# Performance work log

Measured on AMD Instinct MI355X. Metric: run time of the kernel, lower is better.

Reference implementation:

```python
import jax, jax.numpy as jnp
import numpy as np

C = 1.0      # base manifold curvature (Lorentz c)
C_E = 1.0    # expert manifold curvature (all experts init to c=1.0)
K = 1        # n_activated_experts (top-k)
SCALE = 2.0  # LResNet scale for shared-expert combine
EPS = 1e-8


def _lorentz_swiglu(x, W1, W3, W2, c_mid, c_out, prescale):
    """LorentzExpert / LorentzFeedForward: SwiGLU on space coords with Lorentz time lift.
    x: [T, D] (full Lorentz vector). W1,W3: [I-1, D]; W2: [D-1, I]. Returns [T, D]."""
    if prescale:
        x = x * np.float32(np.sqrt(C_E / C))  # x * sqrt(c_expert / c)
    s1 = jax.nn.silu(x @ W1.T)                 # [T, I-1] w1(x, return_space=True)
    s3 = x @ W3.T                              # [T, I-1] w3(x, return_space=True)
    sp = s1 * s3                               # gated space part
    t = jnp.sqrt(jnp.clip((sp * sp).sum(-1, keepdims=True) + c_mid, EPS))
    h = jnp.concatenate([t, sp], axis=-1)      # [T, I] point on expert manifold
    o = h @ W2.T                               # [T, D-1] w2 space output
    ot = jnp.sqrt(jnp.clip((o * o).sum(-1, keepdims=True) + c_out, EPS))
    return jnp.concatenate([ot, o], axis=-1)   # [T, D] on base manifold


def setup_inputs() -> dict:
    key = jax.random.key(0)
    ks = jax.random.split(key, 9)
    T, D, E, I = 2048, 1024, 8, 1024
    x = jax.random.normal(ks[0], (T, D), jnp.float32)
    gate_w = jax.random.normal(ks[1], (E, D - 1), jnp.float32) / np.sqrt(D - 1)
    gate_b = jax.random.normal(ks[2], (E,), jnp.float32) * 0.01
    W1 = jax.random.normal(ks[3], (E, I - 1, D), jnp.float32) / np.sqrt(D)
    W3 = jax.random.normal(ks[4], (E, I - 1, D), jnp.float32) / np.sqrt(D)
    W2 = jax.random.normal(ks[5], (E, D - 1, I), jnp.float32) / np.sqrt(I)
    Ws1 = jax.random.normal(ks[6], (I - 1, D), jnp.float32) / np.sqrt(D)
    Ws3 = jax.random.normal(ks[7], (I - 1, D), jnp.float32) / np.sqrt(D)
    Ws2 = jax.random.normal(ks[8], (D - 1, I), jnp.float32) / np.sqrt(I)
    return {"x": x, "gate_w": gate_w, "gate_b": gate_b, "W1": W1, "W3": W3,
            "W2": W2, "Ws1": Ws1, "Ws3": Ws3, "Ws2": Ws2}


def reference(x, gate_w, gate_b, W1, W3, W2, Ws1, Ws3, Ws2):
    T, D = x.shape
    E = gate_w.shape[0]
    # ---- Gate (softmax scoring, n_groups == 1, route_scale == 1.0) ----
    logits = x[:, 1:] @ gate_w.T                                    # [T, E]
    scores = jax.nn.softmax(logits.astype(jnp.float32), axis=-1)
    biased = scores + gate_b                                        # bias only affects routing
    _, idx = jax.lax.top_k(biased, K)                               # [T, K]
    weights = jnp.take_along_axis(scores, idx, axis=-1).astype(x.dtype)  # [T, K]
    # dense per-token expert gate weights [T, E]
    oh = jax.nn.one_hot(idx, E, dtype=x.dtype)                      # [T, K, E]
    gw = (oh * weights[..., None]).sum(axis=1)                      # [T, E]
    # ---- y init: project(zeros) -> [sqrt(c), 0, ..., 0] ----
    y0 = jnp.concatenate([jnp.full((T, 1), np.sqrt(C), x.dtype),
                          jnp.zeros((T, D - 1), x.dtype)], axis=-1)
    # ---- routed experts (dense reference: every expert on every token, masked combine) ----
    e_out = jax.vmap(lambda w1, w3, w2: _lorentz_swiglu(x, w1, w3, w2, C_E, C, True))(W1, W3, W2)  # [E, T, D]
    y = y0 + jnp.einsum('te,etd->td', gw, e_out)
    # ---- shared expert (LorentzFeedForward, stays on base manifold) ----
    z = _lorentz_swiglu(x, Ws1, Ws3, Ws2, C, C, False)
    # ---- LResNet weighted sum: normalize (z + scale*y) back to manifold ----
    comb = z + SCALE * y
    li = (comb[:, 1:] ** 2).sum(-1, keepdims=True) - comb[:, :1] ** 2  # Lorentz inner <comb,comb>
    out = np.float32(np.sqrt(C)) * comb / jnp.sqrt(jnp.clip(jnp.abs(li), EPS))
    return out
```

## Files before the change

### kernel.cpp

```cpp
#include <hip/hip_runtime.h>

typedef __bf16 bf16;
typedef __attribute__((ext_vector_type(8))) __bf16 bf16x8;
typedef __attribute__((ext_vector_type(4))) float floatx4;

#define TOK 2048
#define DD  1024
#define NE  8
#define S1MAX 48
#define S2MAX 80

#define MFMA16(A,B,C) __builtin_amdgcn_mfma_f32_16x16x32_bf16(A,B,C,0,0,0)

__device__ __forceinline__ void load_lds16(const bf16* g, bf16* l) {
  __builtin_amdgcn_global_load_lds(
      (const __attribute__((address_space(1))) void*)g,
      (__attribute__((address_space(3))) void*)l, 16, 0, 0);
}

#define WBAR(N) asm volatile("s_waitcnt vmcnt(" #N ")\n\ts_barrier" ::: "memory")
#define BARO    asm volatile("s_barrier" ::: "memory")

__device__ __forceinline__ uint4 pack_bf8(float4 a, float4 b) {
  union { bf16 h[8]; uint4 u; } p;
  p.h[0] = (bf16)a.x; p.h[1] = (bf16)a.y; p.h[2] = (bf16)a.z; p.h[3] = (bf16)a.w;
  p.h[4] = (bf16)b.x; p.h[5] = (bf16)b.y; p.h[6] = (bf16)b.z; p.h[7] = (bf16)b.w;
  return p.u;
}

#define NCVT (8*2046 + 2046 + 8*1023 + 1023)
__global__ __launch_bounds__(128) void convert_kernel(
    const float* __restrict__ W1, const float* __restrict__ W3,
    const float* __restrict__ W2, const float* __restrict__ Ws1,
    const float* __restrict__ Ws3, const float* __restrict__ Ws2,
    bf16* __restrict__ w13, bf16* __restrict__ ws13,
    bf16* __restrict__ w2b, bf16* __restrict__ ws2b)
{
  const int r = blockIdx.x, tid = threadIdx.x;
  const float* src; bf16* dst;
  if (r < 8 * 2046) {
    const int e = r / 2046, q = r % 2046;
    src = ((q & 1) ? W3 : W1) + ((size_t)e * 1023 + (q >> 1)) * 1024;
    dst = w13 + (size_t)r * 1024;
// ... 57 lines not shown
    for (int e = 0; e < NE; ++e) lg[e] = red[0][e] + red[1][e] + red[2][e] + red[3][e];
    float m = lg[0];
    for (int e = 1; e < NE; ++e) m = fmaxf(m, lg[e]);
    float ex[NE], s = 0.f;
    for (int e = 0; e < NE; ++e) { ex[e] = expf(lg[e] - m); s += ex[e]; }
    const float inv = 1.f / s;
    int best = 0; float bb = ex[0] * inv + gate_b[0];
    for (int e = 1; e < NE; ++e) {
      const float b = ex[e] * inv + gate_b[e];
      if (b > bb) { bb = b; best = e; }
    }
    eidx[t] = best;
    ewgt[t] = ex[best] * inv;
  }
}

__global__ __launch_bounds__(256) void route_kernel(
    const int* __restrict__ eidx, int* __restrict__ perm,
    int* __restrict__ pos_of, int4* __restrict__ wl1, int* __restrict__ n1,
    int4* __restrict__ wl2, int* __restrict__ n2)
{
  __shared__ int cnt[NE], off[NE], bas[NE + 1];
  const int tid = threadIdx.x;
  if (tid < NE) cnt[tid] = 0;
  __syncthreads();
  for (int t = tid; t < TOK; t += 256) atomicAdd(&cnt[eidx[t]], 1);
  __syncthreads();
  if (tid == 0) {
    int run = 0;
    for (int e = 0; e < NE; ++e) { bas[e] = run; off[e] = run; run += cnt[e]; }
    bas[NE] = run;
    int n = 0;
    for (int e = 0; e < NE; ++e)
      for (int r0 = 0; r0 < cnt[e]; r0 += 128) {
        int rows = cnt[e] - r0; if (rows > 128) rows = 128;
        wl1[n++] = make_int4(bas[e] + r0, rows, e, 0);
      }
    for (int r0 = 0; r0 < TOK; r0 += 128) wl1[n++] = make_int4(r0, 128, NE, 0);
    *n1 = n;
    n = 0;
    for (int e = 0; e < NE; ++e)
      for (int r0 = 0; r0 < cnt[e]; r0 += 64) {
        int rows = cnt[e] - r0; if (rows > 64) rows = 64;
        wl2[n++] = make_int4(bas[e] + r0, rows, e, 0);
      }
    for (int r0 = 0; r0 < TOK; r0 += 64) wl2[n++] = make_int4(r0, 64, NE, 0);
    *n2 = n;
  }
  __syncthreads();
  for (int t = tid; t < TOK; t += 256) {
    const int e = eidx[t];
    const int p = atomicAdd(&off[e], 1);
    perm[p] = t;
    pos_of[t] = p;
  }
}

__global__ __launch_bounds__(256) void mlp1_kernel(
    const bf16* __restrict__ x_bf, const bf16* __restrict__ w13,
    const bf16* __restrict__ ws13,
    const int* __restrict__ perm, const int4* __restrict__ wl,
    const int* __restrict__ wl_n,
    bf16* __restrict__ h_r, bf16* __restrict__ h_s,
    float* __restrict__ ss_r, float* __restrict__ ss_z)
{
  const int bid = blockIdx.x;
  const int slot = bid >> 4, nt = bid & 15;
  if (slot >= *wl_n) return;
  const int4 wle = wl[slot];
  const int mbase = wle.x, rows = wle.y, eid = wle.z;
  const int tid = threadIdx.x;
  const bool routed = (eid < NE);
  const bf16* bmat = routed ? w13 + (size_t)eid * 2046 * 1024 : ws13;
  bf16* hbuf  = routed ? h_r : h_s;
  float* ssbuf = routed ? ss_r : ss_z;

  __shared__ __align__(16) bf16 As[2][128 * 64];
  __shared__ __align__(16) bf16 Bs[2][128 * 64];
  __shared__ int toks[128];
  if (tid < 128) {
    int r = tid < rows ? tid : rows - 1;
    toks[tid] = routed ? perm[mbase + r] : (mbase + r);
  }
  __syncthreads();

  const int wid = tid >> 6, lane = tid & 63;
  const int srow = lane >> 3;
  const int kbg  = (lane & 7) ^ (srow & 7);
  const bf16 *aG0, *aG1, *aG2, *aG3, *bG0, *bG1, *bG2, *bG3;
  int aL0o, aL1o, aL2o, aL3o, bL0o, bL1o, bL2o, bL3o;
  {
    const int r0 = wid * 32;
    aG0 = x_bf + (size_t)toks[r0 +  0 + srow] * 1024 + kbg * 8;
    aG1 = x_bf + (size_t)toks[r0 +  8 + srow] * 1024 + kbg * 8;
    aG2 = x_bf + (size_t)toks[r0 + 16 + srow] * 1024 + kbg * 8;
    aG3 = x_bf + (size_t)toks[r0 + 24 + srow] * 1024 + kbg * 8;
    aL0o = (r0 +  0) * 64; aL1o = (r0 +  8) * 64;
    aL2o = (r0 + 16) * 64; aL3o = (r0 + 24) * 64;
    int b0 = nt * 128 + r0 + 0 + srow;  if (b0 > 2045) b0 = 2045;
    int b1 = nt * 128 + r0 + 8 + srow;  if (b1 > 2045) b1 = 2045;
    int b2 = nt * 128 + r0 + 16 + srow; if (b2 > 2045) b2 = 2045;
    int b3 = nt * 128 + r0 + 24 + srow; if (b3 > 2045) b3 = 2045;
    bG0 = bmat + (size_t)b0 * 1024 + kbg * 8;
    bG1 = bmat + (size_t)b1 * 1024 + kbg * 8;
    bG2 = bmat + (size_t)b2 * 1024 + kbg * 8;
    bG3 = bmat + (size_t)b3 * 1024 + kbg * 8;
    bL0o = (r0 +  0) * 64; bL1o = (r0 +  8) * 64;
    bL2o = (r0 + 16) * 64; bL3o = (r0 + 24) * 64;
  }

  const int lrow = lane & 15, quad = lane >> 4, sw = lane & 7;
  const int wrow = (wid >> 1) * 64, wcol = (wid & 1) * 64;
  int aoff[4], boff[4], koff[2];
#pragma unroll
  for (int mi = 0; mi < 4; ++mi) aoff[mi] = (wrow + mi * 16 + lrow) * 64;
#pragma unroll
  for (int ni = 0; ni < 4; ++ni) boff[ni] = (wcol + ni * 16 + lrow) * 64;
#pragma unroll
  for (int kk = 0; kk < 2; ++kk) koff[kk] = ((kk * 4 + quad) ^ sw) * 8;

  const floatx4 fz = {0.f, 0.f, 0.f, 0.f};
  floatx4 acc[4][4];
#pragma unroll
  for (int mi = 0; mi < 4; ++mi)
#pragma unroll
    for (int ni = 0; ni < 4; ++ni) acc[mi][ni] = fz;

#define STAGE1(KE, BUF) { \
    load_lds16(aG0 + (KE), As[BUF] + aL0o); load_lds16(aG1 + (KE), As[BUF] + aL1o); \
    load_lds16(aG2 + (KE), As[BUF] + aL2o); load_lds16(aG3 + (KE), As[BUF] + aL3o); \
    load_lds16(bG0 + (KE), Bs[BUF] + bL0o); load_lds16(bG1 + (KE), Bs[BUF] + bL1o); \
    load_lds16(bG2 + (KE), Bs[BUF] + bL2o); load_lds16(bG3 + (KE), Bs[BUF] + bL3o); }

#define COMP1(BUF) { \
_Pragma("unroll") \
    for (int kk = 0; kk < 2; ++kk) { \
      bf16x8 av[4], bv[4]; \
_Pragma("unroll") \
      for (int mi = 0; mi < 4; ++mi) av[mi] = *(const bf16x8*)(As[BUF] + aoff[mi] + koff[kk]); \
_Pragma("unroll") \
      for (int ni = 0; ni < 4; ++ni) bv[ni] = *(const bf16x8*)(Bs[BUF] + boff[ni] + koff[kk]); \
_Pragma("unroll") \
      for (int mi = 0; mi < 4; ++mi) \
_Pragma("unroll") \
        for (int ni = 0; ni < 4; ++ni) \
          acc[mi][ni] = MFMA16(av[mi], bv[ni], acc[mi][ni]); \
    } }

  STAGE1(0, 0)
  STAGE1(64, 1)
#pragma unroll 1
  for (int t = 0; t < 7; ++t) {
    const int ke = t * 128;
    WBAR(8); COMP1(0) BARO; STAGE1(ke + 128, 0)
    WBAR(8); COMP1(1) BARO; STAGE1(ke + 192, 1)
  }
  WBAR(8); COMP1(0)
  WBAR(0); COMP1(1)
#undef STAGE1
#undef COMP1

#pragma unroll
  for (int mi = 0; mi < 4; ++mi) {
#pragma unroll
    for (int r = 0; r < 4; ++r) {
      const int row = wrow + mi * 16 + quad * 4 + r;
      const bool rowok = row < rows;
      float ssum = 0.f;
#pragma unroll
      for (int ni = 0; ni < 4; ++ni) {
        const float c = acc[mi][ni][r];
        const float partner = __shfl_xor(c, 1);
        const float s1 = (lane & 1) ? partner : c;
        const float s3 = (lane & 1) ? c : partner;
        const float sp = (s1 / (1.f + __expf(-s1))) * s3;
        const int P = (nt * 128 + wcol + ni * 16 + lrow) >> 1;
        const bool ok = rowok && ((lane & 1) == 0) && (P < 1023);
        if (ok) hbuf[(size_t)(mbase + row) * 1024 + 1 + P] = (bf16)sp;
        ssum += ok ? sp * sp : 0.f;
      }
      ssum += __shfl_xor(ssum, 1);
      ssum += __shfl_xor(ssum, 2);
      ssum += __shfl_xor(ssum, 4);
      ssum += __shfl_xor(ssum, 8);
      if (lrow == 0 && rowok) atomicAdd(ssbuf + mbase + row, ssum);
    }
  }
}

__global__ __launch_bounds__(256) void finalize_t_kernel(
    const float* __restrict__ ss_r, const float* __restrict__ ss_z,
    bf16* __restrict__ h_r, bf16* __restrict__ h_s)
{
  const int i = blockIdx.x * 256 + threadIdx.x;
  if (i < TOK) {
    h_r[(size_t)i * 1024] = (bf16)sqrtf(ss_r[i] + 1.0f);
    h_s[(size_t)i * 1024] = (bf16)sqrtf(ss_z[i] + 1.0f);
  }
}

__global__ __launch_bounds__(256) void mlp2_kernel(
    const bf16* __restrict__ h_r, const bf16* __restrict__ h_s,
    const bf16* __restrict__ w2b, const bf16* __restrict__ ws2b,
    const int4* __restrict__ wl, const int* __restrict__ wl_n,
    float* __restrict__ o_r, float* __restrict__ o_s,
    float* __restrict__ ss_or, float* __restrict__ ss_oz)
{
  const int bid = blockIdx.x;
  const int slot = bid >> 3, nt = bid & 7;
  if (slot >= *wl_n) return;
  const int4 wle = wl[slot];
  const int mbase = wle.x, rows = wle.y, eid = wle.z;
  const int tid = threadIdx.x;
  const bool routed = (eid < NE);
  const bf16* abuf = routed ? h_r : h_s;
  const bf16* bmat = routed ? w2b + (size_t)eid * 1023 * 1024 : ws2b;
  float* obuf  = routed ? o_r : o_s;
  float* ssbuf = routed ? ss_or : ss_oz;
  const int n0 = nt * 128;

  __shared__ __align__(16) bf16 As[2][64 * 64];
  __shared__ __align__(16) bf16 Bs[2][128 * 64];

  const int wid = tid >> 6, lane = tid & 63;
  const int srow = lane >> 3;
  const int kbg  = (lane & 7) ^ (srow & 7);
  const bf16 *aG0, *aG1, *bG0, *bG1, *bG2, *bG3;
  int aL0o, aL1o, bL0o, bL1o, bL2o, bL3o;
  {
    int ra0 = wid * 16 + 0 + srow; if (ra0 >= rows) ra0 = rows - 1;
    int ra1 = wid * 16 + 8 + srow; if (ra1 >= rows) ra1 = rows - 1;
    aG0 = abuf + (size_t)(mbase + ra0) * 1024 + kbg * 8;
    aG1 = abuf + (size_t)(mbase + ra1) * 1024 + kbg * 8;
    aL0o = (wid * 16 + 0) * 64;
    aL1o = (wid * 16 + 8) * 64;
    const int r0 = wid * 32;
    int b0 = n0 + r0 + 0 + srow;  if (b0 > 1022) b0 = 1022;
    int b1 = n0 + r0 + 8 + srow;  if (b1 > 1022) b1 = 1022;
    int b2 = n0 + r0 + 16 + srow; if (b2 > 1022) b2 = 1022;
    int b3 = n0 + r0 + 24 + srow; if (b3 > 1022) b3 = 1022;
    bG0 = bmat + (size_t)b0 * 1024 + kbg * 8;
    bG1 = bmat + (size_t)b1 * 1024 + kbg * 8;
    bG2 = bmat + (size_t)b2 * 1024 + kbg * 8;
    bG3 = bmat + (size_t)b3 * 1024 + kbg * 8;
    bL0o = (r0 +  0) * 64; bL1o = (r0 +  8) * 64;
    bL2o = (r0 + 16) * 64; bL3o = (r0 + 24) * 64;
  }

  const int lrow = lane & 15, quad = lane >> 4, sw = lane & 7;
  const int wrow = (wid >> 1) * 32, wcol = (wid & 1) * 64;
  int aoff[2], boff[4], koff[2];
#pragma unroll
  for (int mi = 0; mi < 2; ++mi) aoff[mi] = (wrow + mi * 16 + lrow) * 64;
#pragma unroll
  for (int ni = 0; ni < 4; ++ni) boff[ni] = (wcol + ni * 16 + lrow) * 64;
#pragma unroll
  for (int kk = 0; kk < 2; ++kk) koff[kk] = ((kk * 4 + quad) ^ sw) * 8;

  const floatx4 fz = {0.f, 0.f, 0.f, 0.f};
  floatx4 acc[2][4];
#pragma unroll
  for (int mi = 0; mi < 2; ++mi)
#pragma unroll
    for (int ni = 0; ni < 4; ++ni) acc[mi][ni] = fz;

#define STAGE2(KE, BUF) { \
    load_lds16(aG0 + (KE), As[BUF] + aL0o); load_lds16(aG1 + (KE), As[BUF] + aL1o); \
    load_lds16(bG0 + (KE), Bs[BUF] + bL0o); load_lds16(bG1 + (KE), Bs[BUF] + bL1o); \
    load_lds16(bG2 + (KE), Bs[BUF] + bL2o); load_lds16(bG3 + (KE), Bs[BUF] + bL3o); }

#define COMP2(BUF) { \
_Pragma("unroll") \
    for (int kk = 0; kk < 2; ++kk) { \
      bf16x8 av[2], bv[4]; \
_Pragma("unroll") \
      for (int mi = 0; mi < 2; ++mi) av[mi] = *(const bf16x8*)(As[BUF] + aoff[mi] + koff[kk]); \
_Pragma("unroll") \
      for (int ni = 0; ni < 4; ++ni) bv[ni] = *(const bf16x8*)(Bs[BUF] + boff[ni] + koff[kk]); \
_Pragma("unroll") \
      for (int mi = 0; mi < 2; ++mi) \
_Pragma("unroll") \
        for (int ni = 0; ni < 4; ++ni) \
          acc[mi][ni] = MFMA16(av[mi], bv[ni], acc[mi][ni]); \
    } }

  STAGE2(0, 0)
  STAGE2(64, 1)
#pragma unroll 1
  for (int t = 0; t < 7; ++t) {
    const int ke = t * 128;
    WBAR(6); COMP2(0) BARO; STAGE2(ke + 128, 0)
    WBAR(6); COMP2(1) BARO; STAGE2(ke + 192, 1)
  }
  WBAR(6); COMP2(0)
  WBAR(0); COMP2(1)
#undef STAGE2
#undef COMP2

#pragma unroll
  for (int mi = 0; mi < 2; ++mi) {
#pragma unroll
    for (int r = 0; r < 4; ++r) {
      const int row = wrow + mi * 16 + quad * 4 + r;
      const bool rowok = row < rows;
      float ssum = 0.f;
#pragma unroll
      for (int ni = 0; ni < 4; ++ni) {
        const float v = acc[mi][ni][r];
        const int n = n0 + wcol + ni * 16 + lrow;
        const bool ok = rowok && (n < 1023);
        if (ok) obuf[(size_t)(mbase + row) * 1024 + n] = v;
        ssum += ok ? v * v : 0.f;
      }
      ssum += __shfl_xor(ssum, 1);
      ssum += __shfl_xor(ssum, 2);
      ssum += __shfl_xor(ssum, 4);
      ssum += __shfl_xor(ssum, 8);
      if (lrow == 0 && rowok) atomicAdd(ssbuf + mbase + row, ssum);
    }
  }
}

__global__ __launch_bounds__(256) void combine_kernel(
    const float* __restrict__ o_r, const float* __restrict__ o_s,
    const float* __restrict__ ss_or, const float* __restrict__ ss_oz,
    const int* __restrict__ pos_of, const float* __restrict__ wgt,
    float* __restrict__ out)
{
  const int t = blockIdx.x, tid = threadIdx.x;
  const int p = pos_of[t];
  const float w = wgt[t];
  const float4 oz = ((const float4*)(o_s + (size_t)t * 1024))[tid];
  const float4 oe = ((const float4*)(o_r + (size_t)p * 1024))[tid];
// ... 35 lines not shown
  const float* Ws2    = (const float*)d_in[8];
  float* out = (float*)d_out;

  char* ws = (char*)d_ws;
  size_t off = 0;
  auto alloc = [&](size_t bytes) {
    void* p = ws + off;
    off += (bytes + 255) & ~(size_t)255;
    return p;
  };
  bf16*  x_bf = (bf16*) alloc((size_t)TOK * 1024 * 2);
  bf16*  h_r  = (bf16*) alloc((size_t)TOK * 1024 * 2);
  bf16*  h_s  = (bf16*) alloc((size_t)TOK * 1024 * 2);
  float* o_r  = (float*)alloc((size_t)TOK * 1024 * 4);
  float* o_s  = (float*)alloc((size_t)TOK * 1024 * 4);
  float* ss   = (float*)alloc((size_t)4 * TOK * 4);
  int*   eidx = (int*)  alloc((size_t)TOK * 4);
  float* ewgt = (float*)alloc((size_t)TOK * 4);
  int*   perm = (int*)  alloc((size_t)TOK * 4);
  int*   posf = (int*)  alloc((size_t)TOK * 4);
  int4*  wl1  = (int4*) alloc((size_t)S1MAX * 16);
  int4*  wl2  = (int4*) alloc((size_t)S2MAX * 16);
  int*   wn   = (int*)  alloc(32);
  bf16*  w13  = (bf16*) alloc((size_t)8 * 2046 * 1024 * 2);
  bf16*  ws13 = (bf16*) alloc((size_t)2046 * 1024 * 2);
  bf16*  w2b  = (bf16*) alloc((size_t)8 * 1023 * 1024 * 2);
  bf16*  ws2b = (bf16*) alloc((size_t)1023 * 1024 * 2);

  float* ss_r  = ss;
  float* ss_z  = ss + TOK;
  float* ss_or = ss + 2 * TOK;
  float* ss_oz = ss + 3 * TOK;

  convert_kernel<<<NCVT, 128, 0, stream>>>(W1, W3, W2, Ws1, Ws3, Ws2,
                                           w13, ws13, w2b, ws2b);
  gate_cvt_kernel<<<TOK, 256, 0, stream>>>(x, gate_w, gate_b, x_bf, eidx, ewgt, ss);
  route_kernel<<<1, 256, 0, stream>>>(eidx, perm, posf, wl1, wn, wl2, wn + 1);
  mlp1_kernel<<<S1MAX * 16, 256, 0, stream>>>(x_bf, w13, ws13, perm, wl1, wn,
                                              h_r, h_s, ss_r, ss_z);
  finalize_t_kernel<<<8, 256, 0, stream>>>(ss_r, ss_z, h_r, h_s);
  mlp2_kernel<<<S2MAX * 8, 256, 0, stream>>>(h_r, h_s, w2b, ws2b, wl2, wn + 1,
                                             o_r, o_s, ss_or, ss_oz);
  combine_kernel<<<TOK, 256, 0, stream>>>(o_r, o_s, ss_or, ss_oz, posf, ewgt, out);
}
```

Measured before the change: 251.5 us.

## Switch GEMM mainloops to BK=32 triple-buffered LDS pipeline without swizzle

Both GEMM kernels now stage K tiles of 32 instead of 64 and rotate through three LDS buffers instead of two, so two loads are in flight while one tile is computed. The XOR swizzle on LDS addressing is removed because each row is now only four 16-byte chunks. Each LDS footprint shrinks, which may allow more blocks per CU, but every K step now has half the MFMA work per barrier, which raises synchronisation overhead. Dropping the swizzle risks LDS bank conflicts.

```diff
diff --git a/kernel.cpp b/kernel.cpp
--- a/kernel.cpp
+++ b/kernel.cpp
@@ -175,8 +175,8 @@
   bf16* hbuf  = routed ? h_r : h_s;
   float* ssbuf = routed ? ss_r : ss_z;
 
-  __shared__ __align__(16) bf16 As[2][128 * 64];
-  __shared__ __align__(16) bf16 Bs[2][128 * 64];
+  __shared__ __align__(16) bf16 As[3][128 * 32];
+  __shared__ __align__(16) bf16 Bs[3][128 * 32];
   __shared__ int toks[128];
   if (tid < 128) {
     int r = tid < rows ? tid : rows - 1;
@@ -185,39 +185,29 @@
   __syncthreads();
 
   const int wid = tid >> 6, lane = tid & 63;
-  const int srow = lane >> 3;
-  const int kbg  = (lane & 7) ^ (srow & 7);
-  const bf16 *aG0, *aG1, *aG2, *aG3, *bG0, *bG1, *bG2, *bG3;
-  int aL0o, aL1o, aL2o, aL3o, bL0o, bL1o, bL2o, bL3o;
+  const int srow  = lane >> 2;
+  const int kslot = lane & 3;
+  const bf16 *aG0, *aG1, *bG0, *bG1;
+  int aL0o, aL1o, bL0o, bL1o;
   {
     const int r0 = wid * 32;
-    aG0 = x_bf + (size_t)toks[r0 +  0 + srow] * 1024 + kbg * 8;
-    aG1 = x_bf + (size_t)toks[r0 +  8 + srow] * 1024 + kbg * 8;
-    aG2 = x_bf + (size_t)toks[r0 + 16 + srow] * 1024 + kbg * 8;
-    aG3 = x_bf + (size_t)toks[r0 + 24 + srow] * 1024 + kbg * 8;
-    aL0o = (r0 +  0) * 64; aL1o = (r0 +  8) * 64;
-    aL2o = (r0 + 16) * 64; aL3o = (r0 + 24) * 64;
-    int b0 = nt * 128 + r0 + 0 + srow;  if (b0 > 2045) b0 = 2045;
-    int b1 = nt * 128 + r0 + 8 + srow;  if (b1 > 2045) b1 = 2045;
-    int b2 = nt * 128 + r0 + 16 + srow; if (b2 > 2045) b2 = 2045;
-    int b3 = nt * 128 + r0 + 24 + srow; if (b3 > 2045) b3 = 2045;
-    bG0 = bmat + (size_t)b0 * 1024 + kbg * 8;
-    bG1 = bmat + (size_t)b1 * 1024 + kbg * 8;
-    bG2 = bmat + (size_t)b2 * 1024 + kbg * 8;
-    bG3 = bmat + (size_t)b3 * 1024 + kbg * 8;
-    bL0o = (r0 +  0) * 64; bL1o = (r0 +  8) * 64;
-    bL2o = (r0 + 16) * 64; bL3o = (r0 + 24) * 64;
-  }
-
-  const int lrow = lane & 15, quad = lane >> 4, sw = lane & 7;
+    aG0 = x_bf + (size_t)toks[r0 +  0 + srow] * 1024 + kslot * 8;
+    aG1 = x_bf + (size_t)toks[r0 + 16 + srow] * 1024 + kslot * 8;
+    aL0o = (r0 +  0) * 32; aL1o = (r0 + 16) * 32;
+    int b0 = nt * 128 + r0 +  0 + srow; if (b0 > 2045) b0 = 2045;
+    int b1 = nt * 128 + r0 + 16 + srow; if (b1 > 2045) b1 = 2045;
+    bG0 = bmat + (size_t)b0 * 1024 + kslot * 8;
+    bG1 = bmat + (size_t)b1 * 1024 + kslot * 8;
+    bL0o = (r0 +  0) * 32; bL1o = (r0 + 16) * 32;
+  }
+
+  const int lrow = lane & 15, quad = lane >> 4;
   const int wrow = (wid >> 1) * 64, wcol = (wid & 1) * 64;
-  int aoff[4], boff[4], koff[2];
-#pragma unroll
-  for (int mi = 0; mi < 4; ++mi) aoff[mi] = (wrow + mi * 16 + lrow) * 64;
-#pragma unroll
-  for (int ni = 0; ni < 4; ++ni) boff[ni] = (wcol + ni * 16 + lrow) * 64;
-#pragma unroll
-  for (int kk = 0; kk < 2; ++kk) koff[kk] = ((kk * 4 + quad) ^ sw) * 8;
+  int aoff[4], boff[4];
+#pragma unroll
+  for (int mi = 0; mi < 4; ++mi) aoff[mi] = (wrow + mi * 16 + lrow) * 32 + quad * 8;
+#pragma unroll
+  for (int ni = 0; ni < 4; ++ni) boff[ni] = (wcol + ni * 16 + lrow) * 32 + quad * 8;
 
   const floatx4 fz = {0.f, 0.f, 0.f, 0.f};
   floatx4 acc[4][4];
@@ -228,34 +218,30 @@
 
 #define STAGE1(KE, BUF) { \
     load_lds16(aG0 + (KE), As[BUF] + aL0o); load_lds16(aG1 + (KE), As[BUF] + aL1o); \
-    load_lds16(aG2 + (KE), As[BUF] + aL2o); load_lds16(aG3 + (KE), As[BUF] + aL3o); \
-    load_lds16(bG0 + (KE), Bs[BUF] + bL0o); load_lds16(bG1 + (KE), Bs[BUF] + bL1o); \
-    load_lds16(bG2 + (KE), Bs[BUF] + bL2o); load_lds16(bG3 + (KE), Bs[BUF] + bL3o); }
+    load_lds16(bG0 + (KE), Bs[BUF] + bL0o); load_lds16(bG1 + (KE), Bs[BUF] + bL1o); }
 
 #define COMP1(BUF) { \
-_Pragma("unroll") \
-    for (int kk = 0; kk < 2; ++kk) { \
-      bf16x8 av[4], bv[4]; \
-_Pragma("unroll") \
-      for (int mi = 0; mi < 4; ++mi) av[mi] = *(const bf16x8*)(As[BUF] + aoff[mi] + koff[kk]); \
-_Pragma("unroll") \
-      for (int ni = 0; ni < 4; ++ni) bv[ni] = *(const bf16x8*)(Bs[BUF] + boff[ni] + koff[kk]); \
-_Pragma("unroll") \
-      for (int mi = 0; mi < 4; ++mi) \
-_Pragma("unroll") \
-        for (int ni = 0; ni < 4; ++ni) \
-          acc[mi][ni] = MFMA16(av[mi], bv[ni], acc[mi][ni]); \
-    } }
+    bf16x8 av[4], bv[4]; \
+_Pragma("unroll") \
+    for (int mi = 0; mi < 4; ++mi) av[mi] = *(const bf16x8*)(As[BUF] + aoff[mi]); \
+_Pragma("unroll") \
+    for (int ni = 0; ni < 4; ++ni) bv[ni] = *(const bf16x8*)(Bs[BUF] + boff[ni]); \
+_Pragma("unroll") \
+    for (int mi = 0; mi < 4; ++mi) \
+_Pragma("unroll") \
+      for (int ni = 0; ni < 4; ++ni) \
+        acc[mi][ni] = MFMA16(av[mi], bv[ni], acc[mi][ni]); }
 
   STAGE1(0, 0)
-  STAGE1(64, 1)
+  STAGE1(32, 1)
 #pragma unroll 1
-  for (int t = 0; t < 7; ++t) {
-    const int ke = t * 128;
-    WBAR(8); COMP1(0) BARO; STAGE1(ke + 128, 0)
-    WBAR(8); COMP1(1) BARO; STAGE1(ke + 192, 1)
-  }
-  WBAR(8); COMP1(0)
+  for (int t = 0; t < 10; ++t) {
+    const int ke = t * 96;
+    WBAR(4); COMP1(0) BARO; STAGE1(ke +  64, 2)
+    WBAR(4); COMP1(1) BARO; STAGE1(ke +  96, 0)
+    WBAR(4); COMP1(2) BARO; STAGE1(ke + 128, 1)
+  }
+  WBAR(4); COMP1(0)
   WBAR(0); COMP1(1)
 #undef STAGE1
 #undef COMP1
@@ -319,43 +305,33 @@
   float* ssbuf = routed ? ss_or : ss_oz;
   const int n0 = nt * 128;
 
-  __shared__ __align__(16) bf16 As[2][64 * 64];
-  __shared__ __align__(16) bf16 Bs[2][128 * 64];
+  __shared__ __align__(16) bf16 As[3][64 * 32];
+  __shared__ __align__(16) bf16 Bs[3][128 * 32];
 
   const int wid = tid >> 6, lane = tid & 63;
-  const int srow = lane >> 3;
-  const int kbg  = (lane & 7) ^ (srow & 7);
-  const bf16 *aG0, *aG1, *bG0, *bG1, *bG2, *bG3;
-  int aL0o, aL1o, bL0o, bL1o, bL2o, bL3o;
+  const int srow  = lane >> 2;
+  const int kslot = lane & 3;
+  const bf16 *aG0, *bG0, *bG1;
+  int aL0o, bL0o, bL1o;
   {
-    int ra0 = wid * 16 + 0 + srow; if (ra0 >= rows) ra0 = rows - 1;
-    int ra1 = wid * 16 + 8 + srow; if (ra1 >= rows) ra1 = rows - 1;
-    aG0 = abuf + (size_t)(mbase + ra0) * 1024 + kbg * 8;
-    aG1 = abuf + (size_t)(mbase + ra1) * 1024 + kbg * 8;
-    aL0o = (wid * 16 + 0) * 64;
-    aL1o = (wid * 16 + 8) * 64;
+    int ra = wid * 16 + srow; if (ra >= rows) ra = rows - 1;
+    aG0 = abuf + (size_t)(mbase + ra) * 1024 + kslot * 8;
+    aL0o = (wid * 16) * 32;
     const int r0 = wid * 32;
-    int b0 = n0 + r0 + 0 + srow;  if (b0 > 1022) b0 = 1022;
-    int b1 = n0 + r0 + 8 + srow;  if (b1 > 1022) b1 = 1022;
-    int b2 = n0 + r0 + 16 + srow; if (b2 > 1022) b2 = 1022;
-    int b3 = n0 + r0 + 24 + srow; if (b3 > 1022) b3 = 1022;
-    bG0 = bmat + (size_t)b0 * 1024 + kbg * 8;
-    bG1 = bmat + (size_t)b1 * 1024 + kbg * 8;
-    bG2 = bmat + (size_t)b2 * 1024 + kbg * 8;
-    bG3 = bmat + (size_t)b3 * 1024 + kbg * 8;
-    bL0o = (r0 +  0) * 64; bL1o = (r0 +  8) * 64;
-    bL2o = (r0 + 16) * 64; bL3o = (r0 + 24) * 64;
-  }
-
-  const int lrow = lane & 15, quad = lane >> 4, sw = lane & 7;
+    int b0 = n0 + r0 +  0 + srow; if (b0 > 1022) b0 = 1022;
+    int b1 = n0 + r0 + 16 + srow; if (b1 > 1022) b1 = 1022;
+    bG0 = bmat + (size_t)b0 * 1024 + kslot * 8;
+    bG1 = bmat + (size_t)b1 * 1024 + kslot * 8;
+    bL0o = (r0 +  0) * 32; bL1o = (r0 + 16) * 32;
+  }
+
+  const int lrow = lane & 15, quad = lane >> 4;
   const int wrow = (wid >> 1) * 32, wcol = (wid & 1) * 64;
-  int aoff[2], boff[4], koff[2];
-#pragma unroll
-  for (int mi = 0; mi < 2; ++mi) aoff[mi] = (wrow + mi * 16 + lrow) * 64;
-#pragma unroll
-  for (int ni = 0; ni < 4; ++ni) boff[ni] = (wcol + ni * 16 + lrow) * 64;
-#pragma unroll
-  for (int kk = 0; kk < 2; ++kk) koff[kk] = ((kk * 4 + quad) ^ sw) * 8;
+  int aoff[2], boff[4];
+#pragma unroll
+  for (int mi = 0; mi < 2; ++mi) aoff[mi] = (wrow + mi * 16 + lrow) * 32 + quad * 8;
+#pragma unroll
+  for (int ni = 0; ni < 4; ++ni) boff[ni] = (wcol + ni * 16 + lrow) * 32 + quad * 8;
 
   const floatx4 fz = {0.f, 0.f, 0.f, 0.f};
   floatx4 acc[2][4];
@@ -365,34 +341,31 @@
     for (int ni = 0; ni < 4; ++ni) acc[mi][ni] = fz;
 
 #define STAGE2(KE, BUF) { \
-    load_lds16(aG0 + (KE), As[BUF] + aL0o); load_lds16(aG1 + (KE), As[BUF] + aL1o); \
-    load_lds16(bG0 + (KE), Bs[BUF] + bL0o); load_lds16(bG1 + (KE), Bs[BUF] + bL1o); \
-    load_lds16(bG2 + (KE), Bs[BUF] + bL2o); load_lds16(bG3 + (KE), Bs[BUF] + bL3o); }
+    load_lds16(aG0 + (KE), As[BUF] + aL0o); \
+    load_lds16(bG0 + (KE), Bs[BUF] + bL0o); load_lds16(bG1 + (KE), Bs[BUF] + bL1o); }
 
 #define COMP2(BUF) { \
-_Pragma("unroll") \
-    for (int kk = 0; kk < 2; ++kk) { \
-      bf16x8 av[2], bv[4]; \
-_Pragma("unroll") \
-      for (int mi = 0; mi < 2; ++mi) av[mi] = *(const bf16x8*)(As[BUF] + aoff[mi] + koff[kk]); \
-_Pragma("unroll") \
-      for (int ni = 0; ni < 4; ++ni) bv[ni] = *(const bf16x8*)(Bs[BUF] + boff[ni] + koff[kk]); \
-_Pragma("unroll") \
-      for (int mi = 0; mi < 2; ++mi) \
-_Pragma("unroll") \
-        for (int ni = 0; ni < 4; ++ni) \
-          acc[mi][ni] = MFMA16(av[mi], bv[ni], acc[mi][ni]); \
-    } }
+    bf16x8 av[2], bv[4]; \
+_Pragma("unroll") \
+    for (int mi = 0; mi < 2; ++mi) av[mi] = *(const bf16x8*)(As[BUF] + aoff[mi]); \
+_Pragma("unroll") \
+    for (int ni = 0; ni < 4; ++ni) bv[ni] = *(const bf16x8*)(Bs[BUF] + boff[ni]); \
+_Pragma("unroll") \
+    for (int mi = 0; mi < 2; ++mi) \
+_Pragma("unroll") \
+      for (int ni = 0; ni < 4; ++ni) \
+        acc[mi][ni] = MFMA16(av[mi], bv[ni], acc[mi][ni]); }
 
   STAGE2(0, 0)
-  STAGE2(64, 1)
+  STAGE2(32, 1)
 #pragma unroll 1
-  for (int t = 0; t < 7; ++t) {
-    const int ke = t * 128;
-    WBAR(6); COMP2(0) BARO; STAGE2(ke + 128, 0)
-    WBAR(6); COMP2(1) BARO; STAGE2(ke + 192, 1)
-  }
-  WBAR(6); COMP2(0)
+  for (int t = 0; t < 10; ++t) {
+    const int ke = t * 96;
+    WBAR(3); COMP2(0) BARO; STAGE2(ke +  64, 2)
+    WBAR(3); COMP2(1) BARO; STAGE2(ke +  96, 0)
+    WBAR(3); COMP2(2) BARO; STAGE2(ke + 128, 1)
+  }
+  WBAR(3); COMP2(0)
   WBAR(0); COMP2(1)
 #undef STAGE2
 #undef COMP2
```

Measured after the change: 261.9 us. 4.1% more time.

## Enlarge mlp1 tile to 256 rows with 512 threads and triple-buffered LDS

Applied to the files above, without the earlier changes.

The first expert MLP kernel now processes 256-token tiles with 8 waves instead of 128-token tiles with 4 waves, so each weight tile loaded from global memory is reused across twice as many rows. The K loop moves from double to triple buffering in dynamic shared memory so loads can run further ahead of compute. Routing work lists are regenerated at 256-row granularity and S1MAX is halved to match. The cost is heavier LDS use per block (about 144KB) and fewer blocks, which lowers occupancy and adds padding waste for small per-expert token counts.

```diff
diff --git a/kernel.cpp b/kernel.cpp
--- a/kernel.cpp
+++ b/kernel.cpp
@@ -7,7 +7,7 @@
 #define TOK 2048
 #define DD  1024
 #define NE  8
-#define S1MAX 48
+#define S1MAX 24
 #define S2MAX 80
 
 #define MFMA16(A,B,C) __builtin_amdgcn_mfma_f32_16x16x32_bf16(A,B,C,0,0,0)
@@ -132,11 +132,11 @@
     bas[NE] = run;
     int n = 0;
     for (int e = 0; e < NE; ++e)
-      for (int r0 = 0; r0 < cnt[e]; r0 += 128) {
-        int rows = cnt[e] - r0; if (rows > 128) rows = 128;
+      for (int r0 = 0; r0 < cnt[e]; r0 += 256) {
+        int rows = cnt[e] - r0; if (rows > 256) rows = 256;
         wl1[n++] = make_int4(bas[e] + r0, rows, e, 0);
       }
-    for (int r0 = 0; r0 < TOK; r0 += 128) wl1[n++] = make_int4(r0, 128, NE, 0);
+    for (int r0 = 0; r0 < TOK; r0 += 256) wl1[n++] = make_int4(r0, 256, NE, 0);
     *n1 = n;
     n = 0;
     for (int e = 0; e < NE; ++e)
@@ -156,7 +156,7 @@
   }
 }
 
-__global__ __launch_bounds__(256) void mlp1_kernel(
+__global__ __launch_bounds__(512) void mlp1_kernel(
     const bf16* __restrict__ x_bf, const bf16* __restrict__ w13,
     const bf16* __restrict__ ws13,
     const int* __restrict__ perm, const int4* __restrict__ wl,
@@ -175,10 +175,11 @@
   bf16* hbuf  = routed ? h_r : h_s;
   float* ssbuf = routed ? ss_r : ss_z;
 
-  __shared__ __align__(16) bf16 As[2][128 * 64];
-  __shared__ __align__(16) bf16 Bs[2][128 * 64];
-  __shared__ int toks[128];
-  if (tid < 128) {
+  extern __shared__ __align__(16) bf16 smem[];
+  bf16* const Asb[3] = {smem, smem + 16384, smem + 32768};
+  bf16* const Bsb[3] = {smem + 49152, smem + 57344, smem + 65536};
+  __shared__ int toks[256];
+  if (tid < 256) {
     int r = tid < rows ? tid : rows - 1;
     toks[tid] = routed ? perm[mbase + r] : (mbase + r);
   }
@@ -187,8 +188,8 @@
   const int wid = tid >> 6, lane = tid & 63;
   const int srow = lane >> 3;
   const int kbg  = (lane & 7) ^ (srow & 7);
-  const bf16 *aG0, *aG1, *aG2, *aG3, *bG0, *bG1, *bG2, *bG3;
-  int aL0o, aL1o, aL2o, aL3o, bL0o, bL1o, bL2o, bL3o;
+  const bf16 *aG0, *aG1, *aG2, *aG3, *bG0, *bG1;
+  int aL0o, aL1o, aL2o, aL3o, bL0o, bL1o;
   {
     const int r0 = wid * 32;
     aG0 = x_bf + (size_t)toks[r0 +  0 + srow] * 1024 + kbg * 8;
@@ -197,16 +198,12 @@
     aG3 = x_bf + (size_t)toks[r0 + 24 + srow] * 1024 + kbg * 8;
     aL0o = (r0 +  0) * 64; aL1o = (r0 +  8) * 64;
     aL2o = (r0 + 16) * 64; aL3o = (r0 + 24) * 64;
-    int b0 = nt * 128 + r0 + 0 + srow;  if (b0 > 2045) b0 = 2045;
-    int b1 = nt * 128 + r0 + 8 + srow;  if (b1 > 2045) b1 = 2045;
-    int b2 = nt * 128 + r0 + 16 + srow; if (b2 > 2045) b2 = 2045;
-    int b3 = nt * 128 + r0 + 24 + srow; if (b3 > 2045) b3 = 2045;
+    const int rb = wid * 16;
+    int b0 = nt * 128 + rb + 0 + srow; if (b0 > 2045) b0 = 2045;
+    int b1 = nt * 128 + rb + 8 + srow; if (b1 > 2045) b1 = 2045;
     bG0 = bmat + (size_t)b0 * 1024 + kbg * 8;
     bG1 = bmat + (size_t)b1 * 1024 + kbg * 8;
-    bG2 = bmat + (size_t)b2 * 1024 + kbg * 8;
-    bG3 = bmat + (size_t)b3 * 1024 + kbg * 8;
-    bL0o = (r0 +  0) * 64; bL1o = (r0 +  8) * 64;
-    bL2o = (r0 + 16) * 64; bL3o = (r0 + 24) * 64;
+    bL0o = (rb + 0) * 64; bL1o = (rb + 8) * 64;
   }
 
   const int lrow = lane & 15, quad = lane >> 4, sw = lane & 7;
@@ -227,19 +224,18 @@
     for (int ni = 0; ni < 4; ++ni) acc[mi][ni] = fz;
 
 #define STAGE1(KE, BUF) { \
-    load_lds16(aG0 + (KE), As[BUF] + aL0o); load_lds16(aG1 + (KE), As[BUF] + aL1o); \
-    load_lds16(aG2 + (KE), As[BUF] + aL2o); load_lds16(aG3 + (KE), As[BUF] + aL3o); \
-    load_lds16(bG0 + (KE), Bs[BUF] + bL0o); load_lds16(bG1 + (KE), Bs[BUF] + bL1o); \
-    load_lds16(bG2 + (KE), Bs[BUF] + bL2o); load_lds16(bG3 + (KE), Bs[BUF] + bL3o); }
+    load_lds16(aG0 + (KE), Asb[BUF] + aL0o); load_lds16(aG1 + (KE), Asb[BUF] + aL1o); \
+    load_lds16(aG2 + (KE), Asb[BUF] + aL2o); load_lds16(aG3 + (KE), Asb[BUF] + aL3o); \
+    load_lds16(bG0 + (KE), Bsb[BUF] + bL0o); load_lds16(bG1 + (KE), Bsb[BUF] + bL1o); }
 
 #define COMP1(BUF) { \
 _Pragma("unroll") \
     for (int kk = 0; kk < 2; ++kk) { \
       bf16x8 av[4], bv[4]; \
 _Pragma("unroll") \
-      for (int mi = 0; mi < 4; ++mi) av[mi] = *(const bf16x8*)(As[BUF] + aoff[mi] + koff[kk]); \
-_Pragma("unroll") \
-      for (int ni = 0; ni < 4; ++ni) bv[ni] = *(const bf16x8*)(Bs[BUF] + boff[ni] + koff[kk]); \
+      for (int mi = 0; mi < 4; ++mi) av[mi] = *(const bf16x8*)(Asb[BUF] + aoff[mi] + koff[kk]); \
+_Pragma("unroll") \
+      for (int ni = 0; ni < 4; ++ni) bv[ni] = *(const bf16x8*)(Bsb[BUF] + boff[ni] + koff[kk]); \
 _Pragma("unroll") \
       for (int mi = 0; mi < 4; ++mi) \
 _Pragma("unroll") \
@@ -250,13 +246,16 @@
   STAGE1(0, 0)
   STAGE1(64, 1)
 #pragma unroll 1
-  for (int t = 0; t < 7; ++t) {
-    const int ke = t * 128;
-    WBAR(8); COMP1(0) BARO; STAGE1(ke + 128, 0)
-    WBAR(8); COMP1(1) BARO; STAGE1(ke + 192, 1)
-  }
-  WBAR(8); COMP1(0)
-  WBAR(0); COMP1(1)
+  for (int t = 0; t < 4; ++t) {
+    const int ke = t * 192;
+    WBAR(6); COMP1(0) BARO; STAGE1(ke + 128, 2)
+    WBAR(6); COMP1(1) BARO; STAGE1(ke + 192, 0)
+    WBAR(6); COMP1(2) BARO; STAGE1(ke + 256, 1)
+  }
+  WBAR(6); COMP1(0) BARO; STAGE1(896, 2)
+  WBAR(6); COMP1(1) BARO; STAGE1(960, 0)
+  WBAR(6); COMP1(2)
+  WBAR(0); COMP1(0)
 #undef STAGE1
 #undef COMP1
 
@@ -500,12 +499,16 @@
   float* ss_or = ss + 2 * TOK;
   float* ss_oz = ss + 3 * TOK;
 
+  const int MLP1_LDS = 3 * (256 * 64 + 128 * 64) * 2;
+  (void)hipFuncSetAttribute((const void*)mlp1_kernel,
+                            hipFuncAttributeMaxDynamicSharedMemorySize, MLP1_LDS);
+
   convert_kernel<<<NCVT, 128, 0, stream>>>(W1, W3, W2, Ws1, Ws3, Ws2,
                                            w13, ws13, w2b, ws2b);
   gate_cvt_kernel<<<TOK, 256, 0, stream>>>(x, gate_w, gate_b, x_bf, eidx, ewgt, ss);
   route_kernel<<<1, 256, 0, stream>>>(eidx, perm, posf, wl1, wn, wl2, wn + 1);
-  mlp1_kernel<<<S1MAX * 16, 256, 0, stream>>>(x_bf, w13, ws13, perm, wl1, wn,
-                                              h_r, h_s, ss_r, ss_z);
+  mlp1_kernel<<<S1MAX * 16, 512, MLP1_LDS, stream>>>(x_bf, w13, ws13, perm, wl1, wn,
+                                                     h_r, h_s, ss_r, ss_z);
   finalize_t_kernel<<<8, 256, 0, stream>>>(ss_r, ss_z, h_r, h_s);
   mlp2_kernel<<<S2MAX * 8, 256, 0, stream>>>(h_r, h_s, w2b, ws2b, wl2, wn + 1,
                                              o_r, o_s, ss_or, ss_oz);
```

Measured after the change: 248.9 us. Within noise of the previous version (-1.0%).

## Enlarge MoE GEMM tiles and reorder block-to-slot mapping for weight reuse

Applied to the files above, without the earlier changes.

mlp1 now runs 512-thread blocks computing 128x256 tiles with dynamic LDS, and mlp2 moves from 64-row to 128-row M tiles, so each block loads fewer weight bytes per output. Block indexing changes from slot-major to slot-minor, so concurrently running blocks share the same N tile of the weights and the matching work-list slots. The route kernel emits 128-row work items for stage 2, and the grid bounds S1MAX and S2MAX shrink to 40. The larger tiles cut the number of blocks and raise register and LDS use per block, which can lower occupancy and leave more padded rows in small expert groups.

```diff
diff --git a/kernel.cpp b/kernel.cpp
--- a/kernel.cpp
+++ b/kernel.cpp
@@ -7,8 +7,8 @@
 #define TOK 2048
 #define DD  1024
 #define NE  8
-#define S1MAX 48
-#define S2MAX 80
+#define S1MAX 40
+#define S2MAX 40
 
 #define MFMA16(A,B,C) __builtin_amdgcn_mfma_f32_16x16x32_bf16(A,B,C,0,0,0)
 
@@ -140,11 +140,11 @@
     *n1 = n;
     n = 0;
     for (int e = 0; e < NE; ++e)
-      for (int r0 = 0; r0 < cnt[e]; r0 += 64) {
-        int rows = cnt[e] - r0; if (rows > 64) rows = 64;
+      for (int r0 = 0; r0 < cnt[e]; r0 += 128) {
+        int rows = cnt[e] - r0; if (rows > 128) rows = 128;
         wl2[n++] = make_int4(bas[e] + r0, rows, e, 0);
       }
-    for (int r0 = 0; r0 < TOK; r0 += 64) wl2[n++] = make_int4(r0, 64, NE, 0);
+    for (int r0 = 0; r0 < TOK; r0 += 128) wl2[n++] = make_int4(r0, 128, NE, 0);
     *n2 = n;
   }
   __syncthreads();
@@ -156,7 +156,7 @@
   }
 }
 
-__global__ __launch_bounds__(256) void mlp1_kernel(
+__global__ __launch_bounds__(512) void mlp1_kernel(
     const bf16* __restrict__ x_bf, const bf16* __restrict__ w13,
     const bf16* __restrict__ ws13,
     const int* __restrict__ perm, const int4* __restrict__ wl,
@@ -165,7 +165,7 @@
     float* __restrict__ ss_r, float* __restrict__ ss_z)
 {
   const int bid = blockIdx.x;
-  const int slot = bid >> 4, nt = bid & 15;
+  const int slot = bid % S1MAX, nt = bid / S1MAX;
   if (slot >= *wl_n) return;
   const int4 wle = wl[slot];
   const int mbase = wle.x, rows = wle.y, eid = wle.z;
@@ -175,8 +175,9 @@
   bf16* hbuf  = routed ? h_r : h_s;
   float* ssbuf = routed ? ss_r : ss_z;
 
-  __shared__ __align__(16) bf16 As[2][128 * 64];
-  __shared__ __align__(16) bf16 Bs[2][128 * 64];
+  extern __shared__ __align__(16) bf16 smem[];
+  bf16* const Asb[2] = {smem, smem + 8192};
+  bf16* const Bsb[2] = {smem + 16384, smem + 32768};
   __shared__ int toks[128];
   if (tid < 128) {
     int r = tid < rows ? tid : rows - 1;
@@ -187,30 +188,28 @@
   const int wid = tid >> 6, lane = tid & 63;
   const int srow = lane >> 3;
   const int kbg  = (lane & 7) ^ (srow & 7);
-  const bf16 *aG0, *aG1, *aG2, *aG3, *bG0, *bG1, *bG2, *bG3;
-  int aL0o, aL1o, aL2o, aL3o, bL0o, bL1o, bL2o, bL3o;
+  const bf16 *aG0, *aG1, *bG0, *bG1, *bG2, *bG3;
+  int aL0o, aL1o, bL0o, bL1o, bL2o, bL3o;
   {
-    const int r0 = wid * 32;
-    aG0 = x_bf + (size_t)toks[r0 +  0 + srow] * 1024 + kbg * 8;
-    aG1 = x_bf + (size_t)toks[r0 +  8 + srow] * 1024 + kbg * 8;
-    aG2 = x_bf + (size_t)toks[r0 + 16 + srow] * 1024 + kbg * 8;
-    aG3 = x_bf + (size_t)toks[r0 + 24 + srow] * 1024 + kbg * 8;
-    aL0o = (r0 +  0) * 64; aL1o = (r0 +  8) * 64;
-    aL2o = (r0 + 16) * 64; aL3o = (r0 + 24) * 64;
-    int b0 = nt * 128 + r0 + 0 + srow;  if (b0 > 2045) b0 = 2045;
-    int b1 = nt * 128 + r0 + 8 + srow;  if (b1 > 2045) b1 = 2045;
-    int b2 = nt * 128 + r0 + 16 + srow; if (b2 > 2045) b2 = 2045;
-    int b3 = nt * 128 + r0 + 24 + srow; if (b3 > 2045) b3 = 2045;
+    const int r0a = wid * 16;
+    aG0 = x_bf + (size_t)toks[r0a + 0 + srow] * 1024 + kbg * 8;
+    aG1 = x_bf + (size_t)toks[r0a + 8 + srow] * 1024 + kbg * 8;
+    aL0o = (r0a + 0) * 64; aL1o = (r0a + 8) * 64;
+    const int r0b = wid * 32;
+    int b0 = nt * 256 + r0b +  0 + srow; if (b0 > 2045) b0 = 2045;
+    int b1 = nt * 256 + r0b +  8 + srow; if (b1 > 2045) b1 = 2045;
+    int b2 = nt * 256 + r0b + 16 + srow; if (b2 > 2045) b2 = 2045;
+    int b3 = nt * 256 + r0b + 24 + srow; if (b3 > 2045) b3 = 2045;
     bG0 = bmat + (size_t)b0 * 1024 + kbg * 8;
     bG1 = bmat + (size_t)b1 * 1024 + kbg * 8;
     bG2 = bmat + (size_t)b2 * 1024 + kbg * 8;
     bG3 = bmat + (size_t)b3 * 1024 + kbg * 8;
-    bL0o = (r0 +  0) * 64; bL1o = (r0 +  8) * 64;
-    bL2o = (r0 + 16) * 64; bL3o = (r0 + 24) * 64;
+    bL0o = (r0b +  0) * 64; bL1o = (r0b +  8) * 64;
+    bL2o = (r0b + 16) * 64; bL3o = (r0b + 24) * 64;
   }
 
   const int lrow = lane & 15, quad = lane >> 4, sw = lane & 7;
-  const int wrow = (wid >> 1) * 64, wcol = (wid & 1) * 64;
+  const int wrow = (wid >> 2) * 64, wcol = (wid & 3) * 64;
   int aoff[4], boff[4], koff[2];
 #pragma unroll
   for (int mi = 0; mi < 4; ++mi) aoff[mi] = (wrow + mi * 16 + lrow) * 64;
@@ -227,19 +226,18 @@
     for (int ni = 0; ni < 4; ++ni) acc[mi][ni] = fz;
 
 #define STAGE1(KE, BUF) { \
-    load_lds16(aG0 + (KE), As[BUF] + aL0o); load_lds16(aG1 + (KE), As[BUF] + aL1o); \
-    load_lds16(aG2 + (KE), As[BUF] + aL2o); load_lds16(aG3 + (KE), As[BUF] + aL3o); \
-    load_lds16(bG0 + (KE), Bs[BUF] + bL0o); load_lds16(bG1 + (KE), Bs[BUF] + bL1o); \
-    load_lds16(bG2 + (KE), Bs[BUF] + bL2o); load_lds16(bG3 + (KE), Bs[BUF] + bL3o); }
+    load_lds16(aG0 + (KE), Asb[BUF] + aL0o); load_lds16(aG1 + (KE), Asb[BUF] + aL1o); \
+    load_lds16(bG0 + (KE), Bsb[BUF] + bL0o); load_lds16(bG1 + (KE), Bsb[BUF] + bL1o); \
+    load_lds16(bG2 + (KE), Bsb[BUF] + bL2o); load_lds16(bG3 + (KE), Bsb[BUF] + bL3o); }
 
 #define COMP1(BUF) { \
 _Pragma("unroll") \
     for (int kk = 0; kk < 2; ++kk) { \
       bf16x8 av[4], bv[4]; \
 _Pragma("unroll") \
-      for (int mi = 0; mi < 4; ++mi) av[mi] = *(const bf16x8*)(As[BUF] + aoff[mi] + koff[kk]); \
-_Pragma("unroll") \
-      for (int ni = 0; ni < 4; ++ni) bv[ni] = *(const bf16x8*)(Bs[BUF] + boff[ni] + koff[kk]); \
+      for (int mi = 0; mi < 4; ++mi) av[mi] = *(const bf16x8*)(Asb[BUF] + aoff[mi] + koff[kk]); \
+_Pragma("unroll") \
+      for (int ni = 0; ni < 4; ++ni) bv[ni] = *(const bf16x8*)(Bsb[BUF] + boff[ni] + koff[kk]); \
 _Pragma("unroll") \
       for (int mi = 0; mi < 4; ++mi) \
 _Pragma("unroll") \
@@ -252,10 +250,10 @@
 #pragma unroll 1
   for (int t = 0; t < 7; ++t) {
     const int ke = t * 128;
-    WBAR(8); COMP1(0) BARO; STAGE1(ke + 128, 0)
-    WBAR(8); COMP1(1) BARO; STAGE1(ke + 192, 1)
-  }
-  WBAR(8); COMP1(0)
+    WBAR(6); COMP1(0) BARO; STAGE1(ke + 128, 0)
+    WBAR(6); COMP1(1) BARO; STAGE1(ke + 192, 1)
+  }
+  WBAR(6); COMP1(0)
   WBAR(0); COMP1(1)
 #undef STAGE1
 #undef COMP1
@@ -274,7 +272,7 @@
         const float s1 = (lane & 1) ? partner : c;
         const float s3 = (lane & 1) ? c : partner;
         const float sp = (s1 / (1.f + __expf(-s1))) * s3;
-        const int P = (nt * 128 + wcol + ni * 16 + lrow) >> 1;
+        const int P = (nt * 256 + wcol + ni * 16 + lrow) >> 1;
         const bool ok = rowok && ((lane & 1) == 0) && (P < 1023);
         if (ok) hbuf[(size_t)(mbase + row) * 1024 + 1 + P] = (bf16)sp;
         ssum += ok ? sp * sp : 0.f;
@@ -307,7 +305,7 @@
     float* __restrict__ ss_or, float* __restrict__ ss_oz)
 {
   const int bid = blockIdx.x;
-  const int slot = bid >> 3, nt = bid & 7;
+  const int slot = bid % S2MAX, nt = bid / S2MAX;
   if (slot >= *wl_n) return;
   const int4 wle = wl[slot];
   const int mbase = wle.x, rows = wle.y, eid = wle.z;
@@ -319,24 +317,28 @@
   float* ssbuf = routed ? ss_or : ss_oz;
   const int n0 = nt * 128;
 
-  __shared__ __align__(16) bf16 As[2][64 * 64];
+  __shared__ __align__(16) bf16 As[2][128 * 64];
   __shared__ __align__(16) bf16 Bs[2][128 * 64];
 
   const int wid = tid >> 6, lane = tid & 63;
   const int srow = lane >> 3;
   const int kbg  = (lane & 7) ^ (srow & 7);
-  const bf16 *aG0, *aG1, *bG0, *bG1, *bG2, *bG3;
-  int aL0o, aL1o, bL0o, bL1o, bL2o, bL3o;
+  const bf16 *aG0, *aG1, *aG2, *aG3, *bG0, *bG1, *bG2, *bG3;
+  int aL0o, aL1o, aL2o, aL3o, bL0o, bL1o, bL2o, bL3o;
   {
-    int ra0 = wid * 16 + 0 + srow; if (ra0 >= rows) ra0 = rows - 1;
-    int ra1 = wid * 16 + 8 + srow; if (ra1 >= rows) ra1 = rows - 1;
+    const int r0 = wid * 32;
+    int ra0 = r0 +  0 + srow; if (ra0 >= rows) ra0 = rows - 1;
+    int ra1 = r0 +  8 + srow; if (ra1 >= rows) ra1 = rows - 1;
+    int ra2 = r0 + 16 + srow; if (ra2 >= rows) ra2 = rows - 1;
+    int ra3 = r0 + 24 + srow; if (ra3 >= rows) ra3 = rows - 1;
     aG0 = abuf + (size_t)(mbase + ra0) * 1024 + kbg * 8;
     aG1 = abuf + (size_t)(mbase + ra1) * 1024 + kbg * 8;
-    aL0o = (wid * 16 + 0) * 64;
-    aL1o = (wid * 16 + 8) * 64;
-    const int r0 = wid * 32;
-    int b0 = n0 + r0 + 0 + srow;  if (b0 > 1022) b0 = 1022;
-    int b1 = n0 + r0 + 8 + srow;  if (b1 > 1022) b1 = 1022;
+    aG2 = abuf + (size_t)(mbase + ra2) * 1024 + kbg * 8;
+    aG3 = abuf + (size_t)(mbase + ra3) * 1024 + kbg * 8;
+    aL0o = (r0 +  0) * 64; aL1o = (r0 +  8) * 64;
+    aL2o = (r0 + 16) * 64; aL3o = (r0 + 24) * 64;
+    int b0 = n0 + r0 +  0 + srow; if (b0 > 1022) b0 = 1022;
+    int b1 = n0 + r0 +  8 + srow; if (b1 > 1022) b1 = 1022;
     int b2 = n0 + r0 + 16 + srow; if (b2 > 1022) b2 = 1022;
     int b3 = n0 + r0 + 24 + srow; if (b3 > 1022) b3 = 1022;
     bG0 = bmat + (size_t)b0 * 1024 + kbg * 8;
@@ -348,37 +350,38 @@
   }
 
   const int lrow = lane & 15, quad = lane >> 4, sw = lane & 7;
-  const int wrow = (wid >> 1) * 32, wcol = (wid & 1) * 64;
-  int aoff[2], boff[4], koff[2];
-#pragma unroll
-  for (int mi = 0; mi < 2; ++mi) aoff[mi] = (wrow + mi * 16 + lrow) * 64;
+  const int wrow = (wid >> 1) * 64, wcol = (wid & 1) * 64;
+  int aoff[4], boff[4], koff[2];
+#pragma unroll
+  for (int mi = 0; mi < 4; ++mi) aoff[mi] = (wrow + mi * 16 + lrow) * 64;
 #pragma unroll
   for (int ni = 0; ni < 4; ++ni) boff[ni] = (wcol + ni * 16 + lrow) * 64;
 #pragma unroll
   for (int kk = 0; kk < 2; ++kk) koff[kk] = ((kk * 4 + quad) ^ sw) * 8;
 
   const floatx4 fz = {0.f, 0.f, 0.f, 0.f};
-  floatx4 acc[2][4];
-#pragma unroll
-  for (int mi = 0; mi < 2; ++mi)
+  floatx4 acc[4][4];
+#pragma unroll
+  for (int mi = 0; mi < 4; ++mi)
 #pragma unroll
     for (int ni = 0; ni < 4; ++ni) acc[mi][ni] = fz;
 
 #define STAGE2(KE, BUF) { \
     load_lds16(aG0 + (KE), As[BUF] + aL0o); load_lds16(aG1 + (KE), As[BUF] + aL1o); \
+    load_lds16(aG2 + (KE), As[BUF] + aL2o); load_lds16(aG3 + (KE), As[BUF] + aL3o); \
     load_lds16(bG0 + (KE), Bs[BUF] + bL0o); load_lds16(bG1 + (KE), Bs[BUF] + bL1o); \
     load_lds16(bG2 + (KE), Bs[BUF] + bL2o); load_lds16(bG3 + (KE), Bs[BUF] + bL3o); }
 
 #define COMP2(BUF) { \
 _Pragma("unroll") \
     for (int kk = 0; kk < 2; ++kk) { \
-      bf16x8 av[2], bv[4]; \
-_Pragma("unroll") \
-      for (int mi = 0; mi < 2; ++mi) av[mi] = *(const bf16x8*)(As[BUF] + aoff[mi] + koff[kk]); \
+      bf16x8 av[4], bv[4]; \
+_Pragma("unroll") \
+      for (int mi = 0; mi < 4; ++mi) av[mi] = *(const bf16x8*)(As[BUF] + aoff[mi] + koff[kk]); \
 _Pragma("unroll") \
       for (int ni = 0; ni < 4; ++ni) bv[ni] = *(const bf16x8*)(Bs[BUF] + boff[ni] + koff[kk]); \
 _Pragma("unroll") \
-      for (int mi = 0; mi < 2; ++mi) \
+      for (int mi = 0; mi < 4; ++mi) \
 _Pragma("unroll") \
         for (int ni = 0; ni < 4; ++ni) \
           acc[mi][ni] = MFMA16(av[mi], bv[ni], acc[mi][ni]); \
@@ -389,16 +392,16 @@
 #pragma unroll 1
   for (int t = 0; t < 7; ++t) {
     const int ke = t * 128;
-    WBAR(6); COMP2(0) BARO; STAGE2(ke + 128, 0)
-    WBAR(6); COMP2(1) BARO; STAGE2(ke + 192, 1)
-  }
-  WBAR(6); COMP2(0)
+    WBAR(8); COMP2(0) BARO; STAGE2(ke + 128, 0)
+    WBAR(8); COMP2(1) BARO; STAGE2(ke + 192, 1)
+  }
+  WBAR(8); COMP2(0)
   WBAR(0); COMP2(1)
 #undef STAGE2
 #undef COMP2
 
 #pragma unroll
-  for (int mi = 0; mi < 2; ++mi) {
+  for (int mi = 0; mi < 4; ++mi) {
 #pragma unroll
     for (int r = 0; r < 4; ++r) {
       const int row = wrow + mi * 16 + quad * 4 + r;
@@ -500,14 +503,18 @@
   float* ss_or = ss + 2 * TOK;
   float* ss_oz = ss + 3 * TOK;
 
+  const int MLP1_LDS = 2 * (128 * 64 + 256 * 64) * 2;
+  (void)hipFuncSetAttribute((const void*)mlp1_kernel,
+                            hipFuncAttributeMaxDynamicSharedMemorySize, MLP1_LDS);
+
   convert_kernel<<<NCVT, 128, 0, stream>>>(W1, W3, W2, Ws1, Ws3, Ws2,
                                            w13, ws13, w2b, ws2b);
   gate_cvt_kernel<<<TOK, 256, 0, stream>>>(x, gate_w, gate_b, x_bf, eidx, ewgt, ss);
   route_kernel<<<1, 256, 0, stream>>>(eidx, perm, posf, wl1, wn, wl2, wn + 1);
-  mlp1_kernel<<<S1MAX * 16, 256, 0, stream>>>(x_bf, w13, ws13, perm, wl1, wn,
-                                              h_r, h_s, ss_r, ss_z);
+  mlp1_kernel<<<8 * S1MAX, 512, MLP1_LDS, stream>>>(x_bf, w13, ws13, perm, wl1, wn,
+                                                    h_r, h_s, ss_r, ss_z);
   finalize_t_kernel<<<8, 256, 0, stream>>>(ss_r, ss_z, h_r, h_s);
-  mlp2_kernel<<<S2MAX * 8, 256, 0, stream>>>(h_r, h_s, w2b, ws2b, wl2, wn + 1,
+  mlp2_kernel<<<8 * S2MAX, 256, 0, stream>>>(h_r, h_s, w2b, ws2b, wl2, wn + 1,
                                              o_r, o_s, ss_or, ss_oz);
   combine_kernel<<<TOK, 256, 0, stream>>>(o_r, o_s, ss_or, ss_oz, posf, ewgt, out);
 }
```

Result: no change. 252.4 us (+0.4%).
